# Kernel tuning notes

Measured on AMD Instinct MI355X. Metric: run time of the kernel, lower is better.

Reference implementation:

```python
import jax, jax.numpy as jnp
import numpy as np

SEQ, BATCH, EMB = 2048, 8, 1024
HEADS, PROJ = 8, 64


def setup_inputs() -> dict:
    key = jax.random.key(0)
    ks = jax.random.split(key, 7)
    x = jax.random.normal(ks[0], (SEQ, BATCH, EMB), dtype=jnp.float32)
    # pz.nn.Linear: pure einsum weight, no bias
    w_in = jax.random.normal(ks[1], (EMB, HEADS, PROJ), dtype=jnp.float32) / np.sqrt(EMB)
    # eqx.nn.GRUCell params: weight_ih (3P, P_in), weight_hh (3P, P), bias (3P,), bias_n (P,)
    w_ih = jax.random.normal(ks[2], (3 * PROJ, PROJ), dtype=jnp.float32) / np.sqrt(PROJ)
    w_hh = jax.random.normal(ks[3], (3 * PROJ, PROJ), dtype=jnp.float32) / np.sqrt(PROJ)
    b_ih = jax.random.normal(ks[4], (3 * PROJ,), dtype=jnp.float32) * 0.01
    b_n = jax.random.normal(ks[5], (PROJ,), dtype=jnp.float32) * 0.01
    w_out = jax.random.normal(ks[6], (HEADS, PROJ, EMB), dtype=jnp.float32) / np.sqrt(HEADS * PROJ)
    return {"x": x, "w_in": w_in, "w_ih": w_ih, "w_hh": w_hh, "b_ih": b_ih, "b_n": b_n, "w_out": w_out}


def reference(x, w_in, w_ih, w_hh, b_ih, b_n, w_out):
    # project_from_embedding: [S,B,E] -> [S,B,H,P]
    xp = jnp.einsum("sbe,ehp->sbhp", x, w_in)

    def step(h, xt):
        # xt, h: [B,H,P]; GRU cell shared across batch and heads
        ig = jnp.einsum("bhp,gp->bhg", xt, w_ih) + b_ih  # [B,H,3P]
        hg = jnp.einsum("bhp,gp->bhg", h, w_hh)
        ir, iz, inn = jnp.split(ig, 3, axis=-1)
        hr, hz, hn = jnp.split(hg, 3, axis=-1)
        r = jax.nn.sigmoid(ir + hr)
        z = jax.nn.sigmoid(iz + hz)
        n = jnp.tanh(inn + r * (hn + b_n))
        h_new = n + z * (h - n)
        return h_new, h_new

    h0 = jnp.zeros((BATCH, HEADS, PROJ), dtype=x.dtype)
    _, ys = jax.lax.scan(step, h0, xp)  # ys: [S,B,H,P]
    # project_to_embedding: [S,B,H,P] -> [S,B,E]
    return jnp.einsum("sbhp,hpe->sbe", ys, w_out)
```

## Files before the change

kernel.cpp:

```cpp
#include <hip/hip_runtime.h>
#include <math.h>

#define SEQ    2048
#define BATCH  8
#define EMB    1024
#define HEADS  8
#define PROJ   64
#define CHAINS 64
#define GATES  192

typedef float f4  __attribute__((ext_vector_type(4)));
typedef short s8v __attribute__((ext_vector_type(8)));
typedef _Float16 h2v __attribute__((ext_vector_type(2)));

#define AS1(p) ((const __attribute__((address_space(1))) void*)(p))
#define AS3(p) ((__attribute__((address_space(3))) void*)(p))

static __device__ __forceinline__ float bf2f(unsigned short u) {
    union { unsigned int i; float f; } c; c.i = ((unsigned int)u) << 16; return c.f;
}
static __device__ __forceinline__ unsigned short f2bf(float f) {
    union { float f; unsigned int i; } c; c.f = f;
    unsigned int u = c.i;
    u += 0x7fffu + ((u >> 16) & 1u);
    return (unsigned short)(u >> 16);
}
static __device__ __forceinline__ float fdot2u(unsigned int a, unsigned int b, float c) {
    union { unsigned int u; h2v h; } ua, ub; ua.u = a; ub.u = b;
    return __builtin_amdgcn_fdot2(ua.h, ub.h, c, false);
}

__global__ __launch_bounds__(256)
void transpose_to_bf16(const float* __restrict__ in, unsigned short* __restrict__ out,
                       int R, int C) {
    __shared__ float tile[32][33];
    const int tx = threadIdx.x & 31, ty = threadIdx.x >> 5;
    const int c0 = blockIdx.x * 32, r0 = blockIdx.y * 32;
#pragma unroll
    for (int i = 0; i < 4; ++i)
        tile[ty + i * 8][tx] = in[(size_t)(r0 + ty + i * 8) * C + c0 + tx];
    __syncthreads();
#pragma unroll
    for (int i = 0; i < 4; ++i)
        out[(size_t)(c0 + ty + i * 8) * R + r0 + tx] = f2bf(tile[tx][ty + i * 8]);
}

__global__ void convert_bf16(const float* __restrict__ in, unsigned short* __restrict__ out, int n) {
    const int i = blockIdx.x * blockDim.x + threadIdx.x;
    if (i < n) out[i] = f2bf(in[i]);
}

__global__ void convert_f16(const float* __restrict__ in, unsigned short* __restrict__ out, int n) {
    const int i = blockIdx.x * blockDim.x + threadIdx.x;
    if (i < n) {
        union { _Float16 h; unsigned short u; } c;
        c.h = (_Float16)in[i];
        out[i] = c.u;
    }
}

template <int BM, int BN, int BK, bool A_F32, typename OutT, bool BIAS, bool PERM>
__global__ __launch_bounds__((BM / 64) * (BN / 64) * 64)
void gemm_mfma(const void* __restrict__ Ap, const unsigned short* __restrict__ BT,
               OutT* __restrict__ C, const float* __restrict__ bias,
               int M, int N, int K) {
    constexpr int NWN = BN / 64;
    constexpr int NW  = (BM / 64) * NWN;
    constexpr int NT  = NW * 64;
    constexpr int KP  = BK + 8;
    __shared__ unsigned short Al[BM * KP];
    __shared__ unsigned short Bl[BN * KP];

    const int t    = threadIdx.x, lane = t & 63, wid = t >> 6;
    const int wm   = (wid / NWN) * 64, wn = (wid % NWN) * 64;
    const int bm   = blockIdx.x * BM, bn = blockIdx.y * BN;
    const int fr   = lane & 15;
    const int fq   = lane >> 4;

    f4 acc[4][4];
#pragma unroll
    for (int m = 0; m < 4; ++m)
#pragma unroll
        for (int n = 0; n < 4; ++n) acc[m][n] = f4{0.f, 0.f, 0.f, 0.f};

    const int nkt = K / BK;
    for (int kt = 0; kt < nkt; ++kt) {
        const int k0 = kt * BK;
        __syncthreads();
        constexpr int CHA = (BM * BK / 8) / NT;
#pragma unroll
        for (int i = 0; i < CHA; ++i) {
            const int ci = t + i * NT;
            const int r = ci / (BK / 8), cc = (ci % (BK / 8)) * 8;
            if constexpr (A_F32) {
                const float* A = (const float*)Ap;
                const float4 u0 = *(const float4*)&A[(size_t)(bm + r) * K + k0 + cc];
                const float4 u1 = *(const float4*)&A[(size_t)(bm + r) * K + k0 + cc + 4];
                s8v w;
                w[0] = (short)f2bf(u0.x); w[1] = (short)f2bf(u0.y);
                w[2] = (short)f2bf(u0.z); w[3] = (short)f2bf(u0.w);
                w[4] = (short)f2bf(u1.x); w[5] = (short)f2bf(u1.y);
                w[6] = (short)f2bf(u1.z); w[7] = (short)f2bf(u1.w);
                *(s8v*)&Al[r * KP + cc] = w;
            } else {
                const unsigned short* A = (const unsigned short*)Ap;
                *(s8v*)&Al[r * KP + cc] = *(const s8v*)&A[(size_t)(bm + r) * K + k0 + cc];
            }
        }
        constexpr int CHB = (BN * BK / 8) / NT;
#pragma unroll
        for (int i = 0; i < CHB; ++i) {
            const int ci = t + i * NT;
            const int r = ci / (BK / 8), cc = (ci % (BK / 8)) * 8;
            *(s8v*)&Bl[r * KP + cc] = *(const s8v*)&BT[(size_t)(bn + r) * K + k0 + cc];
        }
        __syncthreads();
#pragma unroll
        for (int ks = 0; ks < BK / 32; ++ks) {
            s8v av[4], bv[4];
#pragma unroll
            for (int m = 0; m < 4; ++m)
                av[m] = *(const s8v*)&Al[(wm + m * 16 + fr) * KP + ks * 32 + fq * 8];
#pragma unroll
            for (int n = 0; n < 4; ++n)
                bv[n] = *(const s8v*)&Bl[(wn + n * 16 + fr) * KP + ks * 32 + fq * 8];
#pragma unroll
            for (int m = 0; m < 4; ++m)
#pragma unroll
                for (int n = 0; n < 4; ++n)
                    acc[m][n] = __builtin_amdgcn_mfma_f32_16x16x32_bf16(
                        av[m], bv[n], acc[m][n], 0, 0, 0);
        }
    }

#pragma unroll
    for (int n = 0; n < 4; ++n) {
        const int col = bn + wn + n * 16 + fr;
        const float bv = BIAS ? bias[col] : 0.f;
#pragma unroll
        for (int m = 0; m < 4; ++m) {
            const int row0 = bm + wm + m * 16 + fq * 4;
#pragma unroll
            for (int j = 0; j < 4; ++j) {
                const float val = acc[m][n][j] + bv;
                const int row = row0 + j;
                const size_t orow = PERM ? ((size_t)(row & 63) * SEQ + (row >> 6))
                                         : (size_t)row;
                if constexpr (sizeof(OutT) == 4)
                    C[orow * N + col] = val;
                else
                    C[orow * N + col] = f2bf(val);
            }
        }
    }
}

__global__ __launch_bounds__(64, 1)
void gru_scan5(const unsigned short* __restrict__ w_hh16, const float* __restrict__ b_n,
               const unsigned short* __restrict__ ig, unsigned short* __restrict__ ys) {
    const int c = blockIdx.x;
    const int p = threadIdx.x;

    __shared__ unsigned short hl16[PROJ];
    __shared__ uint4 igl[2][384];

    unsigned int wru[32], wzu[32], wnu[32];
#pragma unroll
    for (int q = 0; q < 8; ++q) {
        const uint4 a = *(const uint4*)&w_hh16[(size_t)(0 * PROJ + p) * PROJ + q * 8];
        wru[4*q+0] = a.x; wru[4*q+1] = a.y; wru[4*q+2] = a.z; wru[4*q+3] = a.w;
        const uint4 b = *(const uint4*)&w_hh16[(size_t)(1 * PROJ + p) * PROJ + q * 8];
        wzu[4*q+0] = b.x; wzu[4*q+1] = b.y; wzu[4*q+2] = b.z; wzu[4*q+3] = b.w;
        const uint4 e = *(const uint4*)&w_hh16[(size_t)(2 * PROJ + p) * PROJ + q * 8];
        wnu[4*q+0] = e.x; wnu[4*q+1] = e.y; wnu[4*q+2] = e.z; wnu[4*q+3] = e.w;
    }
    const float bn = b_n[p];

    hl16[p] = 0;
    float hreg = 0.f;

    const char* gbase = (const char*)(ig + (size_t)c * SEQ * GATES);

#pragma unroll
    for (int i = 0; i < 6; ++i)
        __builtin_amdgcn_global_load_lds(AS1(gbase + i * 1024 + p * 16),
                                         AS3((char*)&igl[0][0] + i * 1024), 16, 0, 0);

    unsigned int hw[32];
#pragma unroll
    for (int q = 0; q < 8; ++q) {
        const uint4 v = ((const uint4*)hl16)[q];
        hw[4*q+0] = v.x; hw[4*q+1] = v.y; hw[4*q+2] = v.z; hw[4*q+3] = v.w;
    }

    for (int sb = 0; sb < SEQ; sb += 16) {
        const int buf = (sb >> 4) & 1;
        asm volatile("s_waitcnt vmcnt(0)" ::: "memory");
        __builtin_amdgcn_sched_barrier(0);
        {
            const int nb = (sb + 16 < SEQ) ? sb + 16 : sb;
            const char* src = gbase + (size_t)nb * (GATES * 2);
            char* dst = (char*)&igl[buf ^ 1][0];
#pragma unroll
            for (int i = 0; i < 6; ++i)
                __builtin_amdgcn_global_load_lds(AS1(src + i * 1024 + p * 16),
                                                 AS3(dst + i * 1024), 16, 0, 0);
        }
        __builtin_amdgcn_sched_barrier(0);

#pragma unroll 4
        for (int u = 0; u < 16; ++u) {
            const int s = sb + u;
            const unsigned short* igb = (const unsigned short*)&igl[buf][0] + u * GATES;
            const unsigned short ur = igb[p];
            const unsigned short uz = igb[PROJ + p];
            const unsigned short un = igb[2 * PROJ + p];

            float ar[4] = {0.f,0.f,0.f,0.f}, az[4] = {0.f,0.f,0.f,0.f}, an[4] = {0.f,0.f,0.f,0.f};
#pragma unroll
            for (int i = 0; i < 32; ++i) {
                const unsigned int h2 = hw[i];
                ar[i & 3] = fdot2u(h2, wru[i], ar[i & 3]);
                an[i & 3] = fdot2u(h2, wnu[i], an[i & 3]);
                az[i & 3] = fdot2u(h2, wzu[i], az[i & 3]);
            }
            const float hgr = (ar[0] + ar[1]) + (ar[2] + ar[3]);
            const float hgn = (an[0] + an[1]) + (an[2] + an[3]);
            const float hgz = (az[0] + az[1]) + (az[2] + az[3]);

            const float r = __builtin_amdgcn_rcpf(1.f + __expf(-(bf2f(ur) + hgr)));
            const float z = __builtin_amdgcn_rcpf(1.f + __expf(-(bf2f(uz) + hgz)));
            const float y  = bf2f(un) + r * (hgn + bn);
            const float e2 = __expf(2.f * y);
            const float nn = 1.f - 2.f * __builtin_amdgcn_rcpf(1.f + e2);
            const float hnew = nn + z * (hreg - nn);
            hreg = hnew;

            union { _Float16 h; unsigned short u; } cv; cv.h = (_Float16)hnew;
            hl16[p] = cv.u;
#pragma unroll
            for (int q = 0; q < 8; ++q) {
                const uint4 v = ((const uint4*)hl16)[q];
                hw[4*q+0] = v.x; hw[4*q+1] = v.y; hw[4*q+2] = v.z; hw[4*q+3] = v.w;
            }
            ys[((size_t)s * CHAINS + c) * PROJ + p] = f2bf(hnew);
        }
    }
}

extern "C" void kernel_launch(void* const* d_in, const int* in_sizes, int n_in,
                              void* d_out, int out_size, void* d_ws, size_t ws_size,
                              hipStream_t stream) {
    const float* x     = (const float*)d_in[0];
    const float* w_in  = (const float*)d_in[1];
    const float* w_ih  = (const float*)d_in[2];
    const float* w_hh  = (const float*)d_in[3];
    const float* b_ih  = (const float*)d_in[4];
    const float* b_n   = (const float*)d_in[5];
    const float* w_out = (const float*)d_in[6];
    float* out = (float*)d_out;

    char* ws = (char*)d_ws;
    const size_t xp_bytes  = (size_t)SEQ * CHAINS * PROJ * 2;
    const size_t ig_bytes  = (size_t)SEQ * CHAINS * GATES * 2;
    unsigned short* xp_bf  = (unsigned short*)(ws);
    unsigned short* ysb    = (unsigned short*)(ws);
    unsigned short* ig     = (unsigned short*)(ws + xp_bytes);
    unsigned short* w_inT  = (unsigned short*)(ws + xp_bytes + ig_bytes);
    unsigned short* w_outT = w_inT + (size_t)512 * 1024;
    unsigned short* w_ihb  = w_outT + (size_t)1024 * 512;
    unsigned short* w_hh16 = w_ihb + (size_t)GATES * PROJ;

    transpose_to_bf16<<<dim3(512 / 32, 1024 / 32), 256, 0, stream>>>(w_in, w_inT, 1024, 512);
    transpose_to_bf16<<<dim3(1024 / 32, 512 / 32), 256, 0, stream>>>(w_out, w_outT, 512, 1024);
    convert_bf16<<<(GATES * PROJ + 255) / 256, 256, 0, stream>>>(w_ih, w_ihb, GATES * PROJ);
    convert_f16<<<(GATES * PROJ + 255) / 256, 256, 0, stream>>>(w_hh, w_hh16, GATES * PROJ);

    gemm_mfma<128, 128, 64, true, unsigned short, false, false>
        <<<dim3(16384 / 128, 512 / 128), 256, 0, stream>>>(
            x, w_inT, xp_bf, nullptr, 16384, 512, 1024);

    gemm_mfma<128, 64, 64, false, unsigned short, true, true>
        <<<dim3(131072 / 128, 192 / 64), 128, 0, stream>>>(
            xp_bf, w_ihb, ig, b_ih, 131072, 192, 64);

    gru_scan5<<<CHAINS, 64, 0, stream>>>(w_hh16, b_n, ig, ysb);

    gemm_mfma<128, 128, 64, false, float, false, false>
        <<<dim3(16384 / 128, 1024 / 128), 256, 0, stream>>>(
            ysb, w_outT, out, nullptr, 16384, 1024, 512);
}
```

Measured before the change: 761.9 us.

## Interleave two GRU chains per wavefront to hide recurrent latency

The scan kernel now processes two independent chains per 64-thread block (32 blocks instead of 64), alternating steps of chain A and chain B so that one chain's dot products and transcendentals can overlap the other's LDS round-trip latency. The prefetch wait moves from before the next-block loads to the end of each 16-step block, using a partial vmcnt count. The cost is half as many blocks in flight on the GPU, more registers per thread, and a more fragile counter-based synchronisation for the async LDS loads.

```diff
diff --git a/kernel.cpp b/kernel.cpp
--- a/kernel.cpp
+++ b/kernel.cpp
@@ -156,13 +156,16 @@
 }
 
 __global__ __launch_bounds__(64, 1)
-void gru_scan5(const unsigned short* __restrict__ w_hh16, const float* __restrict__ b_n,
+void gru_scan6(const unsigned short* __restrict__ w_hh16, const float* __restrict__ b_n,
                const unsigned short* __restrict__ ig, unsigned short* __restrict__ ys) {
-    const int c = blockIdx.x;
+    const int blk = blockIdx.x;
+    const int cA = 2 * blk, cB = 2 * blk + 1;
     const int p = threadIdx.x;
 
-    __shared__ unsigned short hl16[PROJ];
-    __shared__ uint4 igl[2][384];
+    __shared__ unsigned short hA16[PROJ];
+    __shared__ unsigned short hB16[PROJ];
+    __shared__ uint4 iglA[2][384];
+    __shared__ uint4 iglB[2][384];
 
     unsigned int wru[32], wzu[32], wnu[32];
 #pragma unroll
@@ -176,75 +179,114 @@
     }
     const float bn = b_n[p];
 
-    hl16[p] = 0;
-    float hreg = 0.f;
-
-    const char* gbase = (const char*)(ig + (size_t)c * SEQ * GATES);
-
-#pragma unroll
-    for (int i = 0; i < 6; ++i)
-        __builtin_amdgcn_global_load_lds(AS1(gbase + i * 1024 + p * 16),
-                                         AS3((char*)&igl[0][0] + i * 1024), 16, 0, 0);
-
-    unsigned int hw[32];
-#pragma unroll
-    for (int q = 0; q < 8; ++q) {
-        const uint4 v = ((const uint4*)hl16)[q];
-        hw[4*q+0] = v.x; hw[4*q+1] = v.y; hw[4*q+2] = v.z; hw[4*q+3] = v.w;
-    }
+    hA16[p] = 0; hB16[p] = 0;
+    float hregA = 0.f, hregB = 0.f;
+    unsigned int hwA[32], hwB[32];
+#pragma unroll
+    for (int i = 0; i < 32; ++i) { hwA[i] = 0u; hwB[i] = 0u; }
+
+    const char* gA = (const char*)(ig + (size_t)cA * SEQ * GATES);
+    const char* gB = (const char*)(ig + (size_t)cB * SEQ * GATES);
+
+#pragma unroll
+    for (int i = 0; i < 6; ++i) {
+        __builtin_amdgcn_global_load_lds(AS1(gA + i * 1024 + p * 16),
+                                         AS3((char*)&iglA[0][0] + i * 1024), 16, 0, 0);
+        __builtin_amdgcn_global_load_lds(AS1(gB + i * 1024 + p * 16),
+                                         AS3((char*)&iglB[0][0] + i * 1024), 16, 0, 0);
+    }
+    asm volatile("s_waitcnt vmcnt(0)" ::: "memory");
 
     for (int sb = 0; sb < SEQ; sb += 16) {
         const int buf = (sb >> 4) & 1;
-        asm volatile("s_waitcnt vmcnt(0)" ::: "memory");
-        __builtin_amdgcn_sched_barrier(0);
         {
             const int nb = (sb + 16 < SEQ) ? sb + 16 : sb;
-            const char* src = gbase + (size_t)nb * (GATES * 2);
-            char* dst = (char*)&igl[buf ^ 1][0];
-#pragma unroll
-            for (int i = 0; i < 6; ++i)
-                __builtin_amdgcn_global_load_lds(AS1(src + i * 1024 + p * 16),
-                                                 AS3(dst + i * 1024), 16, 0, 0);
-        }
-        __builtin_amdgcn_sched_barrier(0);
+            const char* srcA = gA + (size_t)nb * (GATES * 2);
+            const char* srcB = gB + (size_t)nb * (GATES * 2);
+            char* dstA = (char*)&iglA[buf ^ 1][0];
+            char* dstB = (char*)&iglB[buf ^ 1][0];
+#pragma unroll
+            for (int i = 0; i < 6; ++i) {
+                __builtin_amdgcn_global_load_lds(AS1(srcA + i * 1024 + p * 16),
+                                                 AS3(dstA + i * 1024), 16, 0, 0);
+                __builtin_amdgcn_global_load_lds(AS1(srcB + i * 1024 + p * 16),
+                                                 AS3(dstB + i * 1024), 16, 0, 0);
+            }
+        }
 
 #pragma unroll 4
         for (int u = 0; u < 16; ++u) {
             const int s = sb + u;
-            const unsigned short* igb = (const unsigned short*)&igl[buf][0] + u * GATES;
-            const unsigned short ur = igb[p];
-            const unsigned short uz = igb[PROJ + p];
-            const unsigned short un = igb[2 * PROJ + p];
-
-            float ar[4] = {0.f,0.f,0.f,0.f}, az[4] = {0.f,0.f,0.f,0.f}, an[4] = {0.f,0.f,0.f,0.f};
-#pragma unroll
-            for (int i = 0; i < 32; ++i) {
-                const unsigned int h2 = hw[i];
-                ar[i & 3] = fdot2u(h2, wru[i], ar[i & 3]);
-                an[i & 3] = fdot2u(h2, wnu[i], an[i & 3]);
-                az[i & 3] = fdot2u(h2, wzu[i], az[i & 3]);
-            }
-            const float hgr = (ar[0] + ar[1]) + (ar[2] + ar[3]);
-            const float hgn = (an[0] + an[1]) + (an[2] + an[3]);
-            const float hgz = (az[0] + az[1]) + (az[2] + az[3]);
-
-            const float r = __builtin_amdgcn_rcpf(1.f + __expf(-(bf2f(ur) + hgr)));
-            const float z = __builtin_amdgcn_rcpf(1.f + __expf(-(bf2f(uz) + hgz)));
-            const float y  = bf2f(un) + r * (hgn + bn);
-            const float e2 = __expf(2.f * y);
-            const float nn = 1.f - 2.f * __builtin_amdgcn_rcpf(1.f + e2);
-            const float hnew = nn + z * (hreg - nn);
-            hreg = hnew;
-
-            union { _Float16 h; unsigned short u; } cv; cv.h = (_Float16)hnew;
-            hl16[p] = cv.u;
-#pragma unroll
-            for (int q = 0; q < 8; ++q) {
-                const uint4 v = ((const uint4*)hl16)[q];
-                hw[4*q+0] = v.x; hw[4*q+1] = v.y; hw[4*q+2] = v.z; hw[4*q+3] = v.w;
-            }
-            ys[((size_t)s * CHAINS + c) * PROJ + p] = f2bf(hnew);
-        }
+            const unsigned short* ia = (const unsigned short*)&iglA[buf][0] + u * GATES;
+            const unsigned short* ib = (const unsigned short*)&iglB[buf][0] + u * GATES;
+            const unsigned short urA = ia[p], uzA = ia[PROJ + p], unA = ia[2 * PROJ + p];
+            const unsigned short urB = ib[p], uzB = ib[PROJ + p], unB = ib[2 * PROJ + p];
+
+            {
+                float ar[4] = {0.f,0.f,0.f,0.f}, az[4] = {0.f,0.f,0.f,0.f}, an[4] = {0.f,0.f,0.f,0.f};
+#pragma unroll
+                for (int i = 0; i < 32; ++i) {
+                    const unsigned int h2 = hwA[i];
+                    ar[i & 3] = fdot2u(h2, wru[i], ar[i & 3]);
+                    an[i & 3] = fdot2u(h2, wnu[i], an[i & 3]);
+                    az[i & 3] = fdot2u(h2, wzu[i], az[i & 3]);
+                }
+                const float hgr = (ar[0] + ar[1]) + (ar[2] + ar[3]);
+                const float hgn = (an[0] + an[1]) + (an[2] + an[3]);
+                const float hgz = (az[0] + az[1]) + (az[2] + az[3]);
+
+                const float r = __builtin_amdgcn_rcpf(1.f + __expf(-(bf2f(urA) + hgr)));
+                const float z = __builtin_amdgcn_rcpf(1.f + __expf(-(bf2f(uzA) + hgz)));
+                const float y  = bf2f(unA) + r * (hgn + bn);
+                const float e2 = __expf(2.f * y);
+                const float nn = 1.f - 2.f * __builtin_amdgcn_rcpf(1.f + e2);
+                const float hnew = nn + z * (hregA - nn);
+                hregA = hnew;
+
+                union { _Float16 h; unsigned short u; } cv; cv.h = (_Float16)hnew;
+                hA16[p] = cv.u;
+#pragma unroll
+                for (int q = 0; q < 8; ++q) {
+                    const uint4 v = ((const uint4*)hA16)[q];
+                    hwA[4*q+0] = v.x; hwA[4*q+1] = v.y; hwA[4*q+2] = v.z; hwA[4*q+3] = v.w;
+                }
+                __builtin_amdgcn_sched_barrier(0);
+                ys[((size_t)s * CHAINS + cA) * PROJ + p] = f2bf(hnew);
+            }
+
+            {
+                float ar[4] = {0.f,0.f,0.f,0.f}, az[4] = {0.f,0.f,0.f,0.f}, an[4] = {0.f,0.f,0.f,0.f};
+#pragma unroll
+                for (int i = 0; i < 32; ++i) {
+                    const unsigned int h2 = hwB[i];
+                    ar[i & 3] = fdot2u(h2, wru[i], ar[i & 3]);
+                    an[i & 3] = fdot2u(h2, wnu[i], an[i & 3]);
+                    az[i & 3] = fdot2u(h2, wzu[i], az[i & 3]);
+                }
+                const float hgr = (ar[0] + ar[1]) + (ar[2] + ar[3]);
+                const float hgn = (an[0] + an[1]) + (an[2] + an[3]);
+                const float hgz = (az[0] + az[1]) + (az[2] + az[3]);
+
+                const float r = __builtin_amdgcn_rcpf(1.f + __expf(-(bf2f(urB) + hgr)));
+                const float z = __builtin_amdgcn_rcpf(1.f + __expf(-(bf2f(uzB) + hgz)));
+                const float y  = bf2f(unB) + r * (hgn + bn);
+                const float e2 = __expf(2.f * y);
+                const float nn = 1.f - 2.f * __builtin_amdgcn_rcpf(1.f + e2);
+                const float hnew = nn + z * (hregB - nn);
+                hregB = hnew;
+
+                union { _Float16 h; unsigned short u; } cv; cv.h = (_Float16)hnew;
+                hB16[p] = cv.u;
+#pragma unroll
+                for (int q = 0; q < 8; ++q) {
+                    const uint4 v = ((const uint4*)hB16)[q];
+                    hwB[4*q+0] = v.x; hwB[4*q+1] = v.y; hwB[4*q+2] = v.z; hwB[4*q+3] = v.w;
+                }
+                __builtin_amdgcn_sched_barrier(0);
+                ys[((size_t)s * CHAINS + cB) * PROJ + p] = f2bf(hnew);
+            }
+        }
+        asm volatile("s_waitcnt vmcnt(32)" ::: "memory");
     }
 }
 
@@ -284,7 +326,7 @@
         <<<dim3(131072 / 128, 192 / 64), 128, 0, stream>>>(
             xp_bf, w_ihb, ig, b_ih, 131072, 192, 64);
 
-    gru_scan5<<<CHAINS, 64, 0, stream>>>(w_hh16, b_n, ig, ysb);
+    gru_scan6<<<CHAINS / 2, 64, 0, stream>>>(w_hh16, b_n, ig, ysb);
 
     gemm_mfma<128, 128, 64, false, float, false, false>
         <<<dim3(16384 / 128, 1024 / 128), 256, 0, stream>>>(
```

New measurement: 1.335 ms. 75.2% more time.

## Fold exp2 scaling into GRU weights and prefetch gates into registers

Applied to the files above, without the earlier changes.

Pre-scales the r/z gate weights and bias by -log2(e) and the n-gate ones by 2*log2(e), so the scan can call exp2 directly without extra multiplies or negation. Replaces the LDS double-buffered async gate staging with a 4-deep register prefetch read from global memory, and splits the three interleaved dot-product chains into separate loops. This is meant to shorten the serial per-step critical path of the recurrence. The trade-off is that global load latency is now exposed to a short prefetch distance, and there is a small extra precision change from folding the scales before the bf16/f16 rounding.

```diff
diff --git a/kernel.cpp b/kernel.cpp
--- a/kernel.cpp
+++ b/kernel.cpp
@@ -9,12 +9,12 @@
 #define CHAINS 64
 #define GATES  192
 
+#define SRZ (-1.4426950408889634f)
+#define SN  ( 2.8853900817779268f)
+
 typedef float f4  __attribute__((ext_vector_type(4)));
 typedef short s8v __attribute__((ext_vector_type(8)));
 typedef _Float16 h2v __attribute__((ext_vector_type(2)));
-
-#define AS1(p) ((const __attribute__((address_space(1))) void*)(p))
-#define AS3(p) ((__attribute__((address_space(3))) void*)(p))
 
 static __device__ __forceinline__ float bf2f(unsigned short u) {
     union { unsigned int i; float f; } c; c.i = ((unsigned int)u) << 16; return c.f;
@@ -45,18 +45,27 @@
         out[(size_t)(c0 + ty + i * 8) * R + r0 + tx] = f2bf(tile[tx][ty + i * 8]);
 }
 
-__global__ void convert_bf16(const float* __restrict__ in, unsigned short* __restrict__ out, int n) {
+__global__ void convert_wih_scaled(const float* __restrict__ in, unsigned short* __restrict__ out) {
     const int i = blockIdx.x * blockDim.x + threadIdx.x;
-    if (i < n) out[i] = f2bf(in[i]);
-}
-
-__global__ void convert_f16(const float* __restrict__ in, unsigned short* __restrict__ out, int n) {
+    if (i < GATES * PROJ) {
+        const float s = (i < 128 * PROJ) ? SRZ : SN;
+        out[i] = f2bf(in[i] * s);
+    }
+}
+
+__global__ void convert_whh_scaled(const float* __restrict__ in, unsigned short* __restrict__ out) {
     const int i = blockIdx.x * blockDim.x + threadIdx.x;
-    if (i < n) {
+    if (i < GATES * PROJ) {
+        const float s = (i < 128 * PROJ) ? SRZ : SN;
         union { _Float16 h; unsigned short u; } c;
-        c.h = (_Float16)in[i];
+        c.h = (_Float16)(in[i] * s);
         out[i] = c.u;
     }
+}
+
+__global__ void scale_bias(const float* __restrict__ in, float* __restrict__ out) {
+    const int i = threadIdx.x;
+    if (i < GATES) out[i] = in[i] * ((i < 128) ? SRZ : SN);
 }
 
 template <int BM, int BN, int BK, bool A_F32, typename OutT, bool BIAS, bool PERM>
@@ -156,13 +165,12 @@
 }
 
 __global__ __launch_bounds__(64, 1)
-void gru_scan5(const unsigned short* __restrict__ w_hh16, const float* __restrict__ b_n,
+void gru_scan8(const unsigned short* __restrict__ w_hh16, const float* __restrict__ b_n,
                const unsigned short* __restrict__ ig, unsigned short* __restrict__ ys) {
     const int c = blockIdx.x;
     const int p = threadIdx.x;
 
     __shared__ unsigned short hl16[PROJ];
-    __shared__ uint4 igl[2][384];
 
     unsigned int wru[32], wzu[32], wnu[32];
 #pragma unroll
@@ -174,77 +182,64 @@
         const uint4 e = *(const uint4*)&w_hh16[(size_t)(2 * PROJ + p) * PROJ + q * 8];
         wnu[4*q+0] = e.x; wnu[4*q+1] = e.y; wnu[4*q+2] = e.z; wnu[4*q+3] = e.w;
     }
-    const float bn = b_n[p];
-
-    hl16[p] = 0;
+    const float bn2 = b_n[p] * SN;
+
     float hreg = 0.f;
-
-    const char* gbase = (const char*)(ig + (size_t)c * SEQ * GATES);
-
-#pragma unroll
-    for (int i = 0; i < 6; ++i)
-        __builtin_amdgcn_global_load_lds(AS1(gbase + i * 1024 + p * 16),
-                                         AS3((char*)&igl[0][0] + i * 1024), 16, 0, 0);
-
     unsigned int hw[32];
 #pragma unroll
-    for (int q = 0; q < 8; ++q) {
-        const uint4 v = ((const uint4*)hl16)[q];
-        hw[4*q+0] = v.x; hw[4*q+1] = v.y; hw[4*q+2] = v.z; hw[4*q+3] = v.w;
-    }
-
-    for (int sb = 0; sb < SEQ; sb += 16) {
-        const int buf = (sb >> 4) & 1;
-        asm volatile("s_waitcnt vmcnt(0)" ::: "memory");
-        __builtin_amdgcn_sched_barrier(0);
+    for (int k = 0; k < 32; ++k) hw[k] = 0u;
+
+    const unsigned short* igc = ig + (size_t)c * SEQ * GATES + p;
+
+    unsigned short pr[4], pz[4], pn[4];
+#pragma unroll
+    for (int k = 0; k < 4; ++k) {
+        const unsigned short* g = igc + (size_t)k * GATES;
+        pr[k] = g[0]; pz[k] = g[PROJ]; pn[k] = g[2 * PROJ];
+    }
+
+#pragma unroll 4
+    for (int s = 0; s < SEQ; ++s) {
+        const int u = s & 3;
+        const float tr = bf2f(pr[u]);
+        const float tz = bf2f(pz[u]);
+        const float tn = bf2f(pn[u]);
         {
-            const int nb = (sb + 16 < SEQ) ? sb + 16 : sb;
-            const char* src = gbase + (size_t)nb * (GATES * 2);
-            char* dst = (char*)&igl[buf ^ 1][0];
-#pragma unroll
-            for (int i = 0; i < 6; ++i)
-                __builtin_amdgcn_global_load_lds(AS1(src + i * 1024 + p * 16),
-                                                 AS3(dst + i * 1024), 16, 0, 0);
-        }
-        __builtin_amdgcn_sched_barrier(0);
-
-#pragma unroll 4
-        for (int u = 0; u < 16; ++u) {
-            const int s = sb + u;
-            const unsigned short* igb = (const unsigned short*)&igl[buf][0] + u * GATES;
-            const unsigned short ur = igb[p];
-            const unsigned short uz = igb[PROJ + p];
-            const unsigned short un = igb[2 * PROJ + p];
-
-            float ar[4] = {0.f,0.f,0.f,0.f}, az[4] = {0.f,0.f,0.f,0.f}, an[4] = {0.f,0.f,0.f,0.f};
-#pragma unroll
-            for (int i = 0; i < 32; ++i) {
-                const unsigned int h2 = hw[i];
-                ar[i & 3] = fdot2u(h2, wru[i], ar[i & 3]);
-                an[i & 3] = fdot2u(h2, wnu[i], an[i & 3]);
-                az[i & 3] = fdot2u(h2, wzu[i], az[i & 3]);
-            }
-            const float hgr = (ar[0] + ar[1]) + (ar[2] + ar[3]);
-            const float hgn = (an[0] + an[1]) + (an[2] + an[3]);
-            const float hgz = (az[0] + az[1]) + (az[2] + az[3]);
-
-            const float r = __builtin_amdgcn_rcpf(1.f + __expf(-(bf2f(ur) + hgr)));
-            const float z = __builtin_amdgcn_rcpf(1.f + __expf(-(bf2f(uz) + hgz)));
-            const float y  = bf2f(un) + r * (hgn + bn);
-            const float e2 = __expf(2.f * y);
-            const float nn = 1.f - 2.f * __builtin_amdgcn_rcpf(1.f + e2);
-            const float hnew = nn + z * (hreg - nn);
-            hreg = hnew;
-
-            union { _Float16 h; unsigned short u; } cv; cv.h = (_Float16)hnew;
-            hl16[p] = cv.u;
-#pragma unroll
-            for (int q = 0; q < 8; ++q) {
-                const uint4 v = ((const uint4*)hl16)[q];
-                hw[4*q+0] = v.x; hw[4*q+1] = v.y; hw[4*q+2] = v.z; hw[4*q+3] = v.w;
-            }
-            ys[((size_t)s * CHAINS + c) * PROJ + p] = f2bf(hnew);
-        }
+            int sn = s + 4; if (sn > SEQ - 1) sn = SEQ - 1;
+            const unsigned short* g = igc + (size_t)sn * GATES;
+            pr[u] = g[0]; pz[u] = g[PROJ]; pn[u] = g[2 * PROJ];
+        }
+
+        float ar[4] = {0.f, 0.f, 0.f, 0.f};
+#pragma unroll
+        for (int k = 0; k < 32; ++k) ar[k & 3] = fdot2u(hw[k], wru[k], ar[k & 3]);
+        const float hgr = (ar[0] + ar[1]) + (ar[2] + ar[3]);
+
+        float an[4] = {0.f, 0.f, 0.f, 0.f};
+#pragma unroll
+        for (int k = 0; k < 32; ++k) an[k & 3] = fdot2u(hw[k], wnu[k], an[k & 3]);
+        const float hgn = (an[0] + an[1]) + (an[2] + an[3]);
+
+        float az[4] = {0.f, 0.f, 0.f, 0.f};
+#pragma unroll
+        for (int k = 0; k < 32; ++k) az[k & 3] = fdot2u(hw[k], wzu[k], az[k & 3]);
+        const float hgz = (az[0] + az[1]) + (az[2] + az[3]);
+
+        const float r  = __builtin_amdgcn_rcpf(1.f + __builtin_amdgcn_exp2f(tr + hgr));
+        const float z  = __builtin_amdgcn_rcpf(1.f + __builtin_amdgcn_exp2f(tz + hgz));
+        const float y2 = fmaf(r, hgn + bn2, tn);
+        const float nn = fmaf(-2.f, __builtin_amdgcn_rcpf(1.f + __builtin_amdgcn_exp2f(y2)), 1.f);
+        const float hnew = nn + z * (hreg - nn);
+        hreg = hnew;
+
+        union { _Float16 h; unsigned short u; } cv; cv.h = (_Float16)hnew;
+        hl16[p] = cv.u;
+#pragma unroll
+        for (int q = 0; q < 8; ++q) {
+            const uint4 v = ((const uint4*)hl16)[q];
+            hw[4*q+0] = v.x; hw[4*q+1] = v.y; hw[4*q+2] = v.z; hw[4*q+3] = v.w;
+        }
+        ys[((size_t)s * CHAINS + c) * PROJ + p] = f2bf(hnew);
     }
 }
 
@@ -270,11 +265,13 @@
     unsigned short* w_outT = w_inT + (size_t)512 * 1024;
     unsigned short* w_ihb  = w_outT + (size_t)1024 * 512;
     unsigned short* w_hh16 = w_ihb + (size_t)GATES * PROJ;
+    float*          bs     = (float*)(w_hh16 + (size_t)GATES * PROJ);
 
     transpose_to_bf16<<<dim3(512 / 32, 1024 / 32), 256, 0, stream>>>(w_in, w_inT, 1024, 512);
     transpose_to_bf16<<<dim3(1024 / 32, 512 / 32), 256, 0, stream>>>(w_out, w_outT, 512, 1024);
-    convert_bf16<<<(GATES * PROJ + 255) / 256, 256, 0, stream>>>(w_ih, w_ihb, GATES * PROJ);
-    convert_f16<<<(GATES * PROJ + 255) / 256, 256, 0, stream>>>(w_hh, w_hh16, GATES * PROJ);
+    convert_wih_scaled<<<(GATES * PROJ + 255) / 256, 256, 0, stream>>>(w_ih, w_ihb);
+    convert_whh_scaled<<<(GATES * PROJ + 255) / 256, 256, 0, stream>>>(w_hh, w_hh16);
+    scale_bias<<<1, 256, 0, stream>>>(b_ih, bs);
 
     gemm_mfma<128, 128, 64, true, unsigned short, false, false>
         <<<dim3(16384 / 128, 512 / 128), 256, 0, stream>>>(
@@ -282,9 +279,9 @@
 
     gemm_mfma<128, 64, 64, false, unsigned short, true, true>
         <<<dim3(131072 / 128, 192 / 64), 128, 0, stream>>>(
-            xp_bf, w_ihb, ig, b_ih, 131072, 192, 64);
-
-    gru_scan5<<<CHAINS, 64, 0, stream>>>(w_hh16, b_n, ig, ysb);
+            xp_bf, w_ihb, ig, bs, 131072, 192, 64);
+
+    gru_scan8<<<CHAINS, 64, 0, stream>>>(w_hh16, b_n, ig, ysb);
 
     gemm_mfma<128, 128, 64, false, float, false, false>
         <<<dim3(16384 / 128, 1024 / 128), 256, 0, stream>>>(
```

Measured after the change: 734.5 us. -3.6%, faster.
